# Performance work log

Measured on AMD Instinct MI355X. Metric: run time of the kernel, lower is better.

Reference implementation:

```python
import jax, jax.numpy as jnp
import numpy as np

M_PER_GROUP = 16
ITER_NUM = 5
EPS = 1e-3


def _iter_norm_whiten(sigma, iter_num=ITER_NUM):
    """Newton-Schulz iteration for Sigma^{-1/2}. sigma: (G, m, m)."""
    g, m, _ = sigma.shape
    eye = jnp.eye(m, dtype=sigma.dtype)
    # normalize by trace so spectral radius < 1
    trace = jnp.trace(sigma, axis1=1, axis2=2)[:, None, None]  # (G,1,1)
    sigma_n = sigma / trace
    P = jnp.broadcast_to(eye, (g, m, m))
    for _ in range(iter_num):
        P3 = P @ P @ P
        P = 1.5 * P - 0.5 * (P3 @ sigma_n)
    # whitening matrix: Sigma^{-1/2} = P / sqrt(trace)
    return P * jax.lax.rsqrt(trace)


def setup_inputs() -> dict:
    key = jax.random.key(0)
    inputs = jax.random.normal(key, (64, 56, 56, 256), dtype=jnp.float32)
    return {"inputs": inputs}


def reference(inputs) -> jnp.ndarray:
    b, w, h, c = inputs.shape
    group = c // M_PER_GROUP
    # center: channels-first flatten, subtract per-channel batch mean
    x = jnp.transpose(inputs, (3, 0, 1, 2)).reshape(c, -1)  # (c, N)
    m = jnp.mean(x, axis=1, keepdims=True)                  # (c, 1)
    f = x - m
    n = f.shape[1]
    fg = f.reshape(group, M_PER_GROUP, n)                   # (G, m, N)
    # per-group covariance
    cov = jnp.einsum('gmn,gkn->gmk', fg, fg) / n            # (G, m, m)
    eye = jnp.eye(M_PER_GROUP, dtype=inputs.dtype)
    sigma = (1.0 - EPS) * cov + EPS * eye
    wm = _iter_norm_whiten(sigma)                           # (G, m, m)
    # whiten
    f_hat = wm @ fg                                         # (G, m, N)
    decorrelated = f_hat.reshape(c, b, w, h)
    return jnp.transpose(decorrelated, (1, 2, 3, 0))        # (b, w, h, c)
```

## Files before the change

### kernel.cpp

```cpp
#include <hip/hip_runtime.h>


constexpr int CCH = 256;
constexpr float EPSV = 1e-3f;
constexpr int PSTRIDE = 4352;
constexpr int STATBLK = 2048;

typedef float f32x4 __attribute__((ext_vector_type(4)));

#define QB(S, comp) __int_as_float(__builtin_amdgcn_update_dpp( \
    0, __float_as_int(comp), (S) * 0x55, 0xF, 0xF, 1))
#define ROT1(comp) __int_as_float(__builtin_amdgcn_update_dpp( \
    0, __float_as_int(comp), 0x39, 0xF, 0xF, 1))
#define ROT2(comp) __int_as_float(__builtin_amdgcn_update_dpp( \
    0, __float_as_int(comp), 0x4E, 0xF, 0xF, 1))

#define FMA4(C, V, U) \
    { C.x += (V).x * (U); C.y += (V).y * (U); C.z += (V).z * (U); C.w += (V).w * (U); }

#define ACCPOS(V)                                                         \
    {                                                                     \
        ss.x += (V).x; ss.y += (V).y; ss.z += (V).z; ss.w += (V).w;       \
        d0 += (V).x * (V).x; d1 += (V).x * (V).y;                         \
        d2 += (V).x * (V).z; d3 += (V).x * (V).w;                         \
        d4 += (V).y * (V).y; d5 += (V).y * (V).z;                         \
        d6 += (V).y * (V).w; d7 += (V).z * (V).z;                         \
        d8 += (V).z * (V).w; d9 += (V).w * (V).w;                         \
        {                                                                 \
            float4 u;                                                     \
            u.x = ROT1((V).x); u.y = ROT1((V).y);                         \
            u.z = ROT1((V).z); u.w = ROT1((V).w);                         \
            FMA4(mA, u, (V).x) FMA4(mB, u, (V).y)                         \
            FMA4(mC, u, (V).z) FMA4(mD, u, (V).w)                         \
        }                                                                 \
        {                                                                 \
            float4 u;                                                     \
            u.x = ROT2((V).x); u.y = ROT2((V).y);                         \
            u.z = ROT2((V).z); u.w = ROT2((V).w);                         \
            FMA4(nA, u, (V).x) FMA4(nB, u, (V).y)                         \
            FMA4(nC, u, (V).z) FMA4(nD, u, (V).w)                         \
        }                                                                 \
    }

constexpr int SLOTF = 4416;

#define SW(RI, CJ, VAL)  sl[gbase + (RI) * 16 + (CJ)] = (VAL);
#define SWM(RI, CJ, VAL) { sl[gbase + (RI) * 16 + (CJ)] = (VAL); \
                           sl[gbase + (CJ) * 16 + (RI)] = (VAL); }
#define SR(RI, CJ, VAR)  VAR += sl[gbase + (RI) * 16 + (CJ)];

#define SLOT_WRITE()                                                        \
    {                                                                       \
        const int R = 4 * rr, A = 4 * c1, B = 4 * c2;                       \
        SW(R+0, R+0, d0) SWM(R+0, R+1, d1) SWM(R+0, R+2, d2)                \
        SWM(R+0, R+3, d3) SW(R+1, R+1, d4) SWM(R+1, R+2, d5)                \
        SWM(R+1, R+3, d6) SW(R+2, R+2, d7) SWM(R+2, R+3, d8)                \
        SW(R+3, R+3, d9)                                                    \
        SWM(R+0, A+0, mA.x) SWM(R+0, A+1, mA.y) SWM(R+0, A+2, mA.z)         \
        SWM(R+0, A+3, mA.w) SWM(R+1, A+0, mB.x) SWM(R+1, A+1, mB.y)         \
        SWM(R+1, A+2, mB.z) SWM(R+1, A+3, mB.w) SWM(R+2, A+0, mC.x)         \
        SWM(R+2, A+1, mC.y) SWM(R+2, A+2, mC.z) SWM(R+2, A+3, mC.w)         \
        SWM(R+3, A+0, mD.x) SWM(R+3, A+1, mD.y) SWM(R+3, A+2, mD.z)         \
        SWM(R+3, A+3, mD.w)                                                 \
        SW(R+0, B+0, nA.x) SW(R+0, B+1, nA.y) SW(R+0, B+2, nA.z)            \
        SW(R+0, B+3, nA.w) SW(R+1, B+0, nB.x) SW(R+1, B+1, nB.y)            \
        SW(R+1, B+2, nB.z) SW(R+1, B+3, nB.w) SW(R+2, B+0, nC.x)            \
        SW(R+2, B+1, nC.y) SW(R+2, B+2, nC.z) SW(R+2, B+3, nC.w)            \
        SW(R+3, B+0, nD.x) SW(R+3, B+1, nD.y) SW(R+3, B+2, nD.z)            \
        SW(R+3, B+3, nD.w)                                                  \
        sl[4160 + lane * 4 + 0] = ss.x; sl[4160 + lane * 4 + 1] = ss.y;     \
        sl[4160 + lane * 4 + 2] = ss.z; sl[4160 + lane * 4 + 3] = ss.w;     \
    }

#define SLOT_ADD()                                                          \
    {                                                                       \
        const int R = 4 * rr, A = 4 * c1, B = 4 * c2;                       \
        SR(R+0, R+0, d0) SR(R+0, R+1, d1) SR(R+0, R+2, d2)                  \
        SR(R+0, R+3, d3) SR(R+1, R+1, d4) SR(R+1, R+2, d5)                  \
        SR(R+1, R+3, d6) SR(R+2, R+2, d7) SR(R+2, R+3, d8)                  \
        SR(R+3, R+3, d9)                                                    \
        SR(R+0, A+0, mA.x) SR(R+0, A+1, mA.y) SR(R+0, A+2, mA.z)            \
        SR(R+0, A+3, mA.w) SR(R+1, A+0, mB.x) SR(R+1, A+1, mB.y)            \
        SR(R+1, A+2, mB.z) SR(R+1, A+3, mB.w) SR(R+2, A+0, mC.x)            \
        SR(R+2, A+1, mC.y) SR(R+2, A+2, mC.z) SR(R+2, A+3, mC.w)            \
        SR(R+3, A+0, mD.x) SR(R+3, A+1, mD.y) SR(R+3, A+2, mD.z)            \
        SR(R+3, A+3, mD.w)                                                  \
        SR(R+0, B+0, nA.x) SR(R+0, B+1, nA.y) SR(R+0, B+2, nA.z)            \
        SR(R+0, B+3, nA.w) SR(R+1, B+0, nB.x) SR(R+1, B+1, nB.y)            \
        SR(R+1, B+2, nB.z) SR(R+1, B+3, nB.w) SR(R+2, B+0, nC.x)            \
        SR(R+2, B+1, nC.y) SR(R+2, B+2, nC.z) SR(R+2, B+3, nC.w)            \
        SR(R+3, B+0, nD.x) SR(R+3, B+1, nD.y) SR(R+3, B+2, nD.z)            \
        SR(R+3, B+3, nD.w)                                                  \
        ss.x += sl[4160 + lane * 4 + 0]; ss.y += sl[4160 + lane * 4 + 1];   \
        ss.z += sl[4160 + lane * 4 + 2]; ss.w += sl[4160 + lane * 4 + 3];   \
    }

__global__ __launch_bounds__(256) void k_stats(const float* __restrict__ x,
                                               float* __restrict__ partial,
                                               int npos) {
    const int tid = threadIdx.x;
    const int lane = tid & 63;
    const int w = tid >> 6;
    const int wave = blockIdx.x * 4 + w;
    const int nwaves = gridDim.x * 4;
    const int g = lane >> 2;
    const int rr = lane & 3;
    const int c1 = (rr + 1) & 3;
    const int c2 = (rr + 2) & 3;
    const int gbase = g * 260;

    float4 ss = {0.f, 0.f, 0.f, 0.f};
    float d0 = 0.f, d1 = 0.f, d2 = 0.f, d3 = 0.f, d4 = 0.f, d5 = 0.f,
          d6 = 0.f, d7 = 0.f, d8 = 0.f, d9 = 0.f;
    float4 mA = ss, mB = ss, mC = ss, mD = ss;
    float4 nA = ss, nB = ss, nC = ss, nD = ss;

    const float* bx = x + lane * 4;

    int p = wave;
    if (p < npos) {
        float4 va = *reinterpret_cast<const float4*>(bx + (size_t)p * CCH);
        while (true) {
            const int pn = p + nwaves;
            const bool more = pn < npos;
            float4 vn = va;
            if (more) vn = *reinterpret_cast<const float4*>(bx + (size_t)pn * CCH);
            ACCPOS(va);
            if (!more) break;
            p = pn;
            va = vn;
        }
    }

    __shared__ float sl[SLOTF];

    if (w == 1) SLOT_WRITE();
    __syncthreads();
    if (w == 0) SLOT_ADD();
    __syncthreads();
    if (w == 3) SLOT_WRITE();
    __syncthreads();
    if (w == 2) SLOT_ADD();
    __syncthreads();
    if (w == 2) SLOT_WRITE();
    __syncthreads();
    if (w == 0) { SLOT_ADD(); SLOT_WRITE(); }
    __syncthreads();

    float* rec = partial + (size_t)blockIdx.x * PSTRIDE;
    for (int c = tid; c < 256; c += blockDim.x)
        rec[c] = sl[4160 + c];
    for (int e = tid; e < 4096; e += blockDim.x) {
        const int gg = e >> 8, row = (e >> 4) & 15, col = e & 15;
        rec[256 + e] = sl[gg * 260 + row * 16 + col];
    }
}

__global__ __launch_bounds__(256) void k_reduce1(const float* __restrict__ partial,
                                                 float* __restrict__ p2,
                                                 int nblk, int nchunks) {
    const int t = blockIdx.x * blockDim.x + threadIdx.x;
    const int total = nchunks * PSTRIDE;
    if (t >= total) return;
    const int chunk = t / PSTRIDE;
    const int e = t - chunk * PSTRIDE;
    const int r0 = chunk * 64;
    const int rend = (r0 + 64 < nblk) ? r0 + 64 : nblk;
    const float* src = partial + (size_t)r0 * PSTRIDE + e;
    float acc = 0.f;
    for (int r = r0; r < rend; ++r, src += PSTRIDE) acc += *src;
    p2[(size_t)chunk * PSTRIDE + e] = acc;
}

__global__ __launch_bounds__(256) void k_reduce2(const float* __restrict__ p2,
                                                 float* __restrict__ finalv,
                                                 int nchunks) {
    const int e = blockIdx.x * blockDim.x + threadIdx.x;
    if (e >= PSTRIDE) return;
    const float* s = p2 + e;
    float acc = 0.f;
    for (int c = 0; c < nchunks; ++c, s += PSTRIDE) acc += *s;
    finalv[e] = acc;
}

__global__ __launch_bounds__(256) void k_wm(const float* __restrict__ sums,
                                            const float* __restrict__ covs,
                                            float* __restrict__ mean,
                                            float* __restrict__ wm,
                                            float inv_n) {
    const int g = blockIdx.x;
    const int tid = threadIdx.x;
    const int i = tid >> 4;
    const int j = tid & 15;

    __shared__ float mu[16];
    __shared__ float sig[16][17];
    __shared__ float P[16][17];
    __shared__ float T[16][17];
    __shared__ float U[16][17];

    if (tid < 16) {
        float m = sums[g * 16 + tid] * inv_n;
        mu[tid] = m;
        mean[g * 16 + tid] = m;
    }
    __syncthreads();

    const float cov = covs[(g * 16 + i) * 16 + j] * inv_n - mu[i] * mu[j];
    const float s = (1.0f - EPSV) * cov + ((i == j) ? EPSV : 0.0f);
    sig[i][j] = s;
    __syncthreads();

    float tr = 0.f;
#pragma unroll
    for (int k = 0; k < 16; ++k) tr += sig[k][k];
    __syncthreads();

    sig[i][j] = s / tr;
    P[i][j] = (i == j) ? 1.0f : 0.0f;
    __syncthreads();

    for (int it = 0; it < 5; ++it) {
        float a = 0.f;
#pragma unroll
        for (int k = 0; k < 16; ++k) a += P[i][k] * P[k][j];
        T[i][j] = a;
        __syncthreads();

        float b = 0.f;
#pragma unroll
        for (int k = 0; k < 16; ++k) b += T[i][k] * P[k][j];
        U[i][j] = b;
        __syncthreads();

        float c = 0.f;
#pragma unroll
        for (int k = 0; k < 16; ++k) c += U[i][k] * sig[k][j];
        const float pn = 1.5f * P[i][j] - 0.5f * c;
        __syncthreads();
        P[i][j] = pn;
        __syncthreads();
    }

    wm[(g * 16 + i) * 16 + j] = P[i][j] * rsqrtf(tr);
}

__global__ __launch_bounds__(256) void k_whiten(const float* __restrict__ x,
                                                const float* __restrict__ mean,
                                                const float* __restrict__ wm,
                                                float* __restrict__ out,
                                                int npos) {
    const int tid = threadIdx.x;
    const int lane = tid & 63;
    const int wave = blockIdx.x * (blockDim.x >> 6) + (tid >> 6);
    const int nwaves = gridDim.x * (blockDim.x >> 6);
    const int g = lane >> 2;
    const int i0 = (lane & 3) * 4;

    float w[4][16];
    const float* wg = wm + g * 256;
#pragma unroll
    for (int a = 0; a < 4; ++a)
#pragma unroll
        for (int j = 0; j < 16; ++j) w[a][j] = wg[(i0 + a) * 16 + j];

    const float4 mu4 = *reinterpret_cast<const float4*>(mean + lane * 4);
    const float* bx = x + lane * 4;
    float* bo = out + lane * 4;

    int p = wave;
    if (p >= npos) return;
    float4 v = *reinterpret_cast<const float4*>(bx + (size_t)p * CCH);
    while (true) {
        const int pn = p + nwaves;
        const bool more = pn < npos;
        float4 vn = v;
        if (more) vn = *reinterpret_cast<const float4*>(bx + (size_t)pn * CCH);

        v.x -= mu4.x; v.y -= mu4.y; v.z -= mu4.z; v.w -= mu4.w;
        float acc[4] = {0.f, 0.f, 0.f, 0.f};
#define WSTEP(S)                                                         \
        {                                                                \
            const float u0 = QB(S, v.x), u1 = QB(S, v.y),                \
                        u2 = QB(S, v.z), u3 = QB(S, v.w);                \
            _Pragma("unroll")                                            \
            for (int a = 0; a < 4; ++a) {                                \
                acc[a] += w[a][(S) * 4 + 0] * u0 + w[a][(S) * 4 + 1] * u1 \
                        + w[a][(S) * 4 + 2] * u2 + w[a][(S) * 4 + 3] * u3; \
            }                                                            \
        }
        WSTEP(0) WSTEP(1) WSTEP(2) WSTEP(3)
#undef WSTEP
        f32x4 o;
        o.x = acc[0]; o.y = acc[1]; o.z = acc[2]; o.w = acc[3];
        __builtin_nontemporal_store(o, reinterpret_cast<f32x4*>(bo + (size_t)p * CCH));

        if (!more) break;
        p = pn;
        v = vn;
    }
}

extern "C" void kernel_launch(void* const* d_in, const int* in_sizes, int n_in,
                              void* d_out, int out_size, void* d_ws, size_t ws_size,
                              hipStream_t stream) {
    const float* x = (const float*)d_in[0];
    float* out = (float*)d_out;
    float* ws = (float*)d_ws;

    const int total = in_sizes[0];
    const int npos = total / CCH;
    const float inv_n = 1.0f / (float)npos;

    float* finalv = ws;
    float* mean = ws + 4352;
    float* wm = ws + 4608;
    float* partial = ws + 8704;

    long avail = (long)(ws_size / 4) - 8704 - 32 * PSTRIDE;
    int nblk = (int)(avail / PSTRIDE);
    if (nblk > STATBLK) nblk = STATBLK;
    if (nblk < 64) nblk = 64;

    float* p2 = partial + (size_t)nblk * PSTRIDE;

    k_stats<<<nblk, 256, 0, stream>>>(x, partial, npos);
    const int nchunks = (nblk + 63) / 64;
    const int r1threads = nchunks * PSTRIDE;
    k_reduce1<<<(r1threads + 255) / 256, 256, 0, stream>>>(partial, p2, nblk, nchunks);
    k_reduce2<<<(PSTRIDE + 255) / 256, 256, 0, stream>>>(p2, finalv, nchunks);
    k_wm<<<16, 256, 0, stream>>>(finalv, finalv + 256, mean, wm, inv_n);
    k_whiten<<<2048, 256, 0, stream>>>(x, mean, wm, out, npos);
}
```

Measured before the change: 150.3 us.

## Stream stats input through double-buffered LDS async loads and fold reduce2 into k_wm

The stats kernel now gives each wave a contiguous chunk of positions and prefetches four rows at a time into double-buffered LDS using global_load_lds with vmcnt waits, replacing the one-row register prefetch. The block count drops to 1024, which halves the partial buffer and the first reduction. The second reduction kernel is removed and its sum over chunks moves into k_wm, saving one launch. This uses 32KB of LDS per block, which may limit occupancy, and the contiguous per-wave chunks change the global access pattern.

```diff
diff --git a/kernel.cpp b/kernel.cpp
--- a/kernel.cpp
+++ b/kernel.cpp
@@ -4,9 +4,19 @@
 constexpr int CCH = 256;
 constexpr float EPSV = 1e-3f;
 constexpr int PSTRIDE = 4352;
-constexpr int STATBLK = 2048;
+constexpr int STATBLK = 1024;
 
 typedef float f32x4 __attribute__((ext_vector_type(4)));
+typedef unsigned int u32;
+
+__device__ __forceinline__ void gload16(const float* g, float* l) {
+    __builtin_amdgcn_global_load_lds(
+        (const __attribute__((address_space(1))) u32*)g,
+        (__attribute__((address_space(3))) u32*)l, 16, 0, 0);
+}
+
+#define WAIT4 asm volatile("s_waitcnt vmcnt(4)" ::: "memory")
+#define WAIT0 asm volatile("s_waitcnt vmcnt(0)" ::: "memory")
 
 #define QB(S, comp) __int_as_float(__builtin_amdgcn_update_dpp( \
     0, __float_as_int(comp), (S) * 0x55, 0xF, 0xF, 1))
@@ -42,8 +52,6 @@
         }                                                                 \
     }
 
-constexpr int SLOTF = 4416;
-
 #define SW(RI, CJ, VAL)  sl[gbase + (RI) * 16 + (CJ)] = (VAL);
 #define SWM(RI, CJ, VAL) { sl[gbase + (RI) * 16 + (CJ)] = (VAL); \
                            sl[gbase + (CJ) * 16 + (RI)] = (VAL); }
@@ -95,13 +103,31 @@
         ss.z += sl[4160 + lane * 4 + 2]; ss.w += sl[4160 + lane * 4 + 3];   \
     }
 
-__global__ __launch_bounds__(256) void k_stats(const float* __restrict__ x,
-                                               float* __restrict__ partial,
-                                               int npos) {
+#define ISSUE(BUF, C)                                                       \
+    {                                                                       \
+        const float* gp = x + (size_t)(start + 4 * (C)) * CCH + lane * 4;   \
+        gload16(gp,           (BUF));                                       \
+        gload16(gp + CCH,     (BUF) + 256);                                 \
+        gload16(gp + 2 * CCH, (BUF) + 512);                                 \
+        gload16(gp + 3 * CCH, (BUF) + 768);                                 \
+    }
+
+#define PROC(BUF)                                                           \
+    {                                                                       \
+        const float4 v0 = *reinterpret_cast<const float4*>((BUF) + lane * 4);        \
+        const float4 v1 = *reinterpret_cast<const float4*>((BUF) + 256 + lane * 4);  \
+        const float4 v2 = *reinterpret_cast<const float4*>((BUF) + 512 + lane * 4);  \
+        const float4 v3 = *reinterpret_cast<const float4*>((BUF) + 768 + lane * 4);  \
+        ACCPOS(v0); ACCPOS(v1); ACCPOS(v2); ACCPOS(v3);                     \
+    }
+
+__global__ __launch_bounds__(256, 4) void k_stats(const float* __restrict__ x,
+                                                  float* __restrict__ partial,
+                                                  int npos) {
     const int tid = threadIdx.x;
     const int lane = tid & 63;
     const int w = tid >> 6;
-    const int wave = blockIdx.x * 4 + w;
+    const int wid = blockIdx.x * 4 + w;
     const int nwaves = gridDim.x * 4;
     const int g = lane >> 2;
     const int rr = lane & 3;
@@ -115,24 +141,43 @@
     float4 mA = ss, mB = ss, mC = ss, mD = ss;
     float4 nA = ss, nB = ss, nC = ss, nD = ss;
 
-    const float* bx = x + lane * 4;
-
-    int p = wave;
-    if (p < npos) {
-        float4 va = *reinterpret_cast<const float4*>(bx + (size_t)p * CCH);
-        while (true) {
-            const int pn = p + nwaves;
-            const bool more = pn < npos;
-            float4 vn = va;
-            if (more) vn = *reinterpret_cast<const float4*>(bx + (size_t)pn * CCH);
-            ACCPOS(va);
-            if (!more) break;
-            p = pn;
-            va = vn;
+    __shared__ float lds[8192];
+    float* b0 = &lds[w * 2048];
+    float* b1 = b0 + 1024;
+
+    const int cpw = (npos + nwaves - 1) / nwaves;
+    const int start = wid * cpw;
+    const int end = (start + cpw < npos) ? start + cpw : npos;
+    const int n = (end > start) ? end - start : 0;
+    const int nf4 = n >> 2;
+
+    if (nf4 >= 2) {
+        ISSUE(b0, 0);
+        ISSUE(b1, 1);
+        int i = 0;
+        for (; i + 2 < nf4; ++i) {
+            WAIT4;
+            float* bb = (i & 1) ? b1 : b0;
+            PROC(bb);
+            ISSUE(bb, i + 2);
         }
-    }
-
-    __shared__ float sl[SLOTF];
+        WAIT4;
+        PROC(((i & 1) ? b1 : b0));
+        ++i;
+        WAIT0;
+        PROC(((i & 1) ? b1 : b0));
+    } else if (nf4 == 1) {
+        ISSUE(b0, 0);
+        WAIT0;
+        PROC(b0);
+    }
+    for (int q = start + 4 * nf4; q < end; ++q) {
+        const float4 v = *reinterpret_cast<const float4*>(x + (size_t)q * CCH + lane * 4);
+        ACCPOS(v);
+    }
+
+    float* sl = lds;
+    __syncthreads();
 
     if (w == 1) SLOT_WRITE();
     __syncthreads();
@@ -172,19 +217,8 @@
     p2[(size_t)chunk * PSTRIDE + e] = acc;
 }
 
-__global__ __launch_bounds__(256) void k_reduce2(const float* __restrict__ p2,
-                                                 float* __restrict__ finalv,
-                                                 int nchunks) {
-    const int e = blockIdx.x * blockDim.x + threadIdx.x;
-    if (e >= PSTRIDE) return;
-    const float* s = p2 + e;
-    float acc = 0.f;
-    for (int c = 0; c < nchunks; ++c, s += PSTRIDE) acc += *s;
-    finalv[e] = acc;
-}
-
-__global__ __launch_bounds__(256) void k_wm(const float* __restrict__ sums,
-                                            const float* __restrict__ covs,
+__global__ __launch_bounds__(256) void k_wm(const float* __restrict__ p2,
+                                            int nchunks,
                                             float* __restrict__ mean,
                                             float* __restrict__ wm,
                                             float inv_n) {
@@ -199,14 +233,22 @@
     __shared__ float T[16][17];
     __shared__ float U[16][17];
 
+    float cs = 0.f;
+    {
+        const float* s = p2 + 256 + g * 256 + i * 16 + j;
+        for (int c = 0; c < nchunks; ++c, s += PSTRIDE) cs += *s;
+    }
     if (tid < 16) {
-        float m = sums[g * 16 + tid] * inv_n;
+        float ms = 0.f;
+        const float* s = p2 + g * 16 + tid;
+        for (int c = 0; c < nchunks; ++c, s += PSTRIDE) ms += *s;
+        const float m = ms * inv_n;
         mu[tid] = m;
         mean[g * 16 + tid] = m;
     }
     __syncthreads();
 
-    const float cov = covs[(g * 16 + i) * 16 + j] * inv_n - mu[i] * mu[j];
+    const float cov = cs * inv_n - mu[i] * mu[j];
     const float s = (1.0f - EPSV) * cov + ((i == j) ? EPSV : 0.0f);
     sig[i][j] = s;
     __syncthreads();
@@ -312,12 +354,11 @@
     const int npos = total / CCH;
     const float inv_n = 1.0f / (float)npos;
 
-    float* finalv = ws;
     float* mean = ws + 4352;
     float* wm = ws + 4608;
     float* partial = ws + 8704;
 
-    long avail = (long)(ws_size / 4) - 8704 - 32 * PSTRIDE;
+    long avail = (long)(ws_size / 4) - 8704 - 16 * PSTRIDE;
     int nblk = (int)(avail / PSTRIDE);
     if (nblk > STATBLK) nblk = STATBLK;
     if (nblk < 64) nblk = 64;
@@ -328,7 +369,6 @@
     const int nchunks = (nblk + 63) / 64;
     const int r1threads = nchunks * PSTRIDE;
     k_reduce1<<<(r1threads + 255) / 256, 256, 0, stream>>>(partial, p2, nblk, nchunks);
-    k_reduce2<<<(PSTRIDE + 255) / 256, 256, 0, stream>>>(p2, finalv, nchunks);
-    k_wm<<<16, 256, 0, stream>>>(finalv, finalv + 256, mean, wm, inv_n);
+    k_wm<<<16, 256, 0, stream>>>(p2, nchunks, mean, wm, inv_n);
     k_whiten<<<2048, 256, 0, stream>>>(x, mean, wm, out, npos);
 }
```

After: 138.3 us (median of 2 runs). 1.09x faster.
